# Performance work log

Hardware: AMD Instinct MI355X
Metric: run time of the kernel (lower is better)

## Reference

```python
import jax, jax.numpy as jnp
import numpy as np

X_DIM, H_DIM, Y_DIM, ROLLOUT = 256, 2048, 256, 4096


def setup_inputs() -> dict:
    key = jax.random.key(0)
    ks = jax.random.split(key, 6)
    inp = {
        "x": jax.random.normal(ks[0], (1, ROLLOUT, X_DIM), dtype=jnp.float32),
        "h": jnp.zeros((H_DIM,), dtype=jnp.float32),
        "Wc": jax.random.normal(ks[1], (X_DIM + H_DIM, H_DIM), dtype=jnp.float32) * 0.01,
        "Wu": jax.random.normal(ks[2], (X_DIM + H_DIM, H_DIM), dtype=jnp.float32) * 0.01,
        "Wr": jax.random.normal(ks[3], (X_DIM + H_DIM, H_DIM), dtype=jnp.float32) * 0.01,
        "bc": jnp.zeros((H_DIM,), dtype=jnp.float32),
        "bu": jnp.zeros((H_DIM,), dtype=jnp.float32),
        "br": jnp.zeros((H_DIM,), dtype=jnp.float32),
        "Wh_y": jax.random.normal(ks[4], (H_DIM, Y_DIM), dtype=jnp.float32) * 0.01,
        "by": jnp.zeros((Y_DIM,), dtype=jnp.float32),
    }
    return inp


def reference(x, h, Wc, Wu, Wr, bc, bu, br, Wh_y, by):
    xs = x[0]  # [T, x_dim]

    def step(hid, xt):
        xc = jnp.concatenate([xt, hid])                      # [x_dim + h_dim]
        Lu = jax.nn.sigmoid(xc @ Wu + bu)                    # update gate
        Lr = jax.nn.sigmoid(xc @ Wr + br)                    # reset gate
        xr = jnp.concatenate([xt, hid * Lr])
        c_tilda = jnp.tanh(xr @ Wc + bc)
        h_new = c_tilda * Lu + hid * (1.0 - Lu)
        y = h_new @ Wh_y + by
        return h_new, y

    h_fin, ys = jax.lax.scan(step, h, xs)  # ys: [T, y_dim]
    return ys, h_fin
```

## Files before the change

kernel.cpp:

```cpp
#include <hip/hip_runtime.h>
#include <hip/hip_bf16.h>

#define TSTEPS 4096
#define XD 256
#define HD 2048
#define YD 256
#define KD 2304
#define NWG 256
#define NT 512

#define WU_OFF 0
#define WR_OFF (8*KD*2)
#define WC_OFF (16*KD*2)
#define WY_OFF (24*KD*2)
#define HBUF_OFF (WY_OFF + HD*4)
#define ZBUF_OFF (HBUF_OFF + HD*4)
#define RED_OFF (ZBUF_OFF + HD*4)
#define LDS_BYTES (RED_OFF + 256)

#define HGO_U32 0
#define RGO_U32 2048
#define HB0_OFF 16384
#define HB1_OFF 49152
#define RB0_OFF 81920
#define RB1_OFF 114688
#define WS_ZERO_BYTES 147456
#define LSTRIDE 32

__device__ __forceinline__ float bflo(unsigned u){ return __uint_as_float(u << 16); }
__device__ __forceinline__ float bfhi(unsigned u){ return __uint_as_float(u & 0xffff0000u); }
__device__ __forceinline__ unsigned short f2bf(float f){
  unsigned b = __float_as_uint(f);
  b += 0x7fffu + ((b >> 16) & 1u);
  return (unsigned short)(b >> 16);
}
__device__ __forceinline__ float sigmoidf_(float x){ return 1.0f / (1.0f + __expf(-x)); }

__device__ __forceinline__ void storetag(float* p, float v, unsigned tag){
  unsigned b = (__float_as_uint(v) & ~3u) | tag;
  __hip_atomic_store((unsigned*)p, b, __ATOMIC_RELAXED, __HIP_MEMORY_SCOPE_AGENT);
}
__device__ __forceinline__ void flagst(unsigned* p, unsigned v){
  __hip_atomic_store(p, v, __ATOMIC_RELAXED, __HIP_MEMORY_SCOPE_AGENT);
}
__device__ __forceinline__ void spinflag(const unsigned* p, unsigned epoch, long* budget){
  while (__hip_atomic_load(p, __ATOMIC_RELAXED, __HIP_MEMORY_SCOPE_AGENT) < epoch) {
    if (--(*budget) < 0) break;
    __builtin_amdgcn_s_sleep(1);
  }
}

__device__ __forceinline__ void polline32(const float4* p, unsigned tag, long* budget,
                                          float4& r0, float4& r1){
  for (;;) {
    asm volatile("global_load_dwordx4 %0, %2, off sc1\n\t"
                 "global_load_dwordx4 %1, %2, off offset:16 sc1\n\t"
                 "s_waitcnt vmcnt(0)"
                 : "=v"(r0), "=v"(r1) : "v"(p) : "memory");
    unsigned m = (__float_as_uint(r0.x)^tag) | (__float_as_uint(r0.y)^tag)
               | (__float_as_uint(r0.z)^tag) | (__float_as_uint(r0.w)^tag)
               | (__float_as_uint(r1.x)^tag) | (__float_as_uint(r1.y)^tag)
               | (__float_as_uint(r1.z)^tag) | (__float_as_uint(r1.w)^tag);
    if ((m & 3u) == 0u) return;
    if (--(*budget) < 0) return;
    __builtin_amdgcn_s_sleep(1);
  }
}

__device__ __forceinline__ float4 cohload16(const float4* p){
  float4 r;
  asm volatile("global_load_dwordx4 %0, %1, off sc1\n\t"
               "s_waitcnt vmcnt(0)"
               : "=v"(r) : "v"(p) : "memory");
  return r;
}

template<int I0, int I1, int STRIDE>
__device__ __forceinline__ void dotacc(const float* v, const unsigned short* wcol,
                                       int lane, float4& acc){
  #pragma unroll
  for (int i = I0; i < I1; ++i) {
    int k = 4 * (lane + STRIDE * i);
    float4 vv = *(const float4*)(v + k);
    uint2  wq = *(const uint2*)(wcol + k);
    acc.x = fmaf(vv.x, bflo(wq.x), acc.x);
    acc.y = fmaf(vv.y, bfhi(wq.x), acc.y);
    acc.z = fmaf(vv.z, bflo(wq.y), acc.z);
    acc.w = fmaf(vv.w, bfhi(wq.y), acc.w);
  }
}
__device__ __forceinline__ void xpart(const float4 xq, const unsigned short* wcol,
                                      int l6, float4& acc){
  uint2 wq = *(const uint2*)(wcol + 4*l6);
  acc.x = fmaf(xq.x, bflo(wq.x), acc.x);
  acc.y = fmaf(xq.y, bfhi(wq.x), acc.y);
  acc.z = fmaf(xq.z, bflo(wq.y), acc.z);
  acc.w = fmaf(xq.w, bfhi(wq.y), acc.w);
}
__device__ __forceinline__ float redux64(float4 a){
  float s = (a.x + a.y) + (a.z + a.w);
  s += __shfl_xor(s, 32); s += __shfl_xor(s, 16); s += __shfl_xor(s, 8);
  s += __shfl_xor(s, 4);  s += __shfl_xor(s, 2);  s += __shfl_xor(s, 1);
  return s;
}

extern "C" __global__ void __launch_bounds__(NT)
gru_persistent(const float* __restrict__ x,  const float* __restrict__ h0,
               const float* __restrict__ Wc, const float* __restrict__ Wu,
               const float* __restrict__ Wr, const float* __restrict__ bc,
               const float* __restrict__ bu, const float* __restrict__ br,
               const float* __restrict__ Wy, const float* __restrict__ by,
               float* __restrict__ out, unsigned* wsu)
{
  extern __shared__ char smem[];
  unsigned short* wuS = (unsigned short*)(smem + WU_OFF);
  unsigned short* wrS = (unsigned short*)(smem + WR_OFF);
  unsigned short* wcS = (unsigned short*)(smem + WC_OFF);
  float* wyS   = (float*)(smem + WY_OFF);
  float* hbufS = (float*)(smem + HBUF_OFF);
  float* zbufS = (float*)(smem + ZBUF_OFF);
  float* red   = (float*)(smem + RED_OFF);

  unsigned* hgo = wsu + HGO_U32;
  unsigned* rgo = wsu + RGO_U32;
  float* hb[2] = { (float*)((char*)wsu + HB0_OFF), (float*)((char*)wsu + HB1_OFF) };
  float* rb[2] = { (float*)((char*)wsu + RB0_OFF), (float*)((char*)wsu + RB1_OFF) };

  const int wg = blockIdx.x, tid = threadIdx.x;
  const int col0 = 8 * wg;

  for (int idx = tid; idx < 8*KD; idx += NT) {
    int c = idx & 7, k = idx >> 3;
    size_t g = (size_t)k * HD + col0 + c;
    wuS[c*KD + k] = f2bf(Wu[g]);
    wrS[c*KD + k] = f2bf(Wr[g]);
    wcS[c*KD + k] = f2bf(Wc[g]);
  }
  for (int k = tid; k < HD; k += NT) wyS[k] = Wy[(size_t)k * YD + wg];
  if (tid < 8) {
    red[16+tid] = bu[col0+tid];
    red[24+tid] = br[col0+tid];
    red[32+tid] = bc[col0+tid];
    red[56+tid] = h0[col0+tid];
  }
  if (tid == 0) red[40] = by[wg];
  __syncthreads();

  long budget = 20000000;

  const int w  = tid >> 6, l6 = tid & 63;
  const int goline = ((wg & 7) << 3) + w;
  const int sw = tid >> 1, half = tid & 1;
  const int gidx = sw * (LSTRIDE/4) + half;
  const unsigned short* ucol = wuS + w * KD;
  const unsigned short* rcol = wrS + w * KD;
  const unsigned short* ccol = wcS + w * KD;

  float4 xq = ((const float4*)x)[l6];
  float ureg = 0.f;

  auto window = [&](int t){
    float4 au = make_float4(0.f, 0.f, 0.f, 0.f);
    xpart(xq, ucol, l6, au);
    dotacc<1, 9, 64>(hbufS - XD, ucol, l6, au);
    ureg = sigmoidf_(redux64(au) + red[16 + w]);
    int k = 256 * w + 4 * l6;
    float4 hv4 = *(const float4*)(hbufS + k);
    float4 wy4 = *(const float4*)(wyS + k);
    float ys = fmaf(hv4.x, wy4.x, fmaf(hv4.y, wy4.y, fmaf(hv4.z, wy4.z, hv4.w * wy4.w)));
    ys += __shfl_xor(ys, 32); ys += __shfl_xor(ys, 16); ys += __shfl_xor(ys, 8);
    ys += __shfl_xor(ys, 4);  ys += __shfl_xor(ys, 2);  ys += __shfl_xor(ys, 1);
    if (l6 == 0) red[8 + w] = ys;
    if (t + 1 < TSTEPS) xq = ((const float4*)(x + (size_t)(t+1) * XD))[l6];
  };

  for (int t = 0; t < TSTEPS; ++t) {
    float4 a1 = make_float4(0.f, 0.f, 0.f, 0.f);
    xpart(xq, rcol, l6, a1);

    if (t == 0) {
      ((float4*)hbufS)[tid] = ((const float4*)h0)[tid];
      __syncthreads();
    } else if (wg == 0) {
      if (tid < NWG) {
        float4 r0, r1;
        polline32((const float4*)hb[(t+1)&1] + tid*(LSTRIDE/4),
                  (unsigned)(t & 3), &budget, r0, r1);
        ((float4*)hbufS)[2*tid]   = r0;
        ((float4*)hbufS)[2*tid+1] = r1;
      }
      __syncthreads();
      if (tid < 64) flagst(hgo + tid*32, (unsigned)t);
    } else {
      if (l6 == 0) spinflag(hgo + goline*32, (unsigned)t, &budget);
      float4 hv = cohload16((const float4*)hb[(t+1)&1] + gidx);
      ((float4*)hbufS)[tid] = hv;
      __syncthreads();
    }

    dotacc<1, 9, 64>(hbufS - XD, rcol, l6, a1);
    {
      float s = redux64(a1);
      if (l6 == 0)
        storetag(rb[t&1] + wg*LSTRIDE + w,
                 sigmoidf_(s + red[24 + w]) * red[56 + w],
                 (unsigned)((t+1) & 3));
    }

    float4 a2 = make_float4(0.f, 0.f, 0.f, 0.f);
    xpart(xq, ccol, l6, a2);

    if (wg == 0) {
      if (tid < NWG) {
        float4 r0, r1;
        polline32((const float4*)rb[t&1] + tid*(LSTRIDE/4),
                  (unsigned)((t+1) & 3), &budget, r0, r1);
        ((float4*)zbufS)[2*tid]   = r0;
        ((float4*)zbufS)[2*tid+1] = r1;
      }
      __syncthreads();
      if (tid < 64) flagst(rgo + tid*32, (unsigned)(t+1));
      window(t);
      __syncthreads();
    } else {
      window(t);
      if (l6 == 0) spinflag(rgo + goline*32, (unsigned)(t+1), &budget);
      float4 rv = cohload16((const float4*)rb[t&1] + gidx);
      ((float4*)zbufS)[tid] = rv;
      __syncthreads();
    }

    if (tid == 0 && t > 0) {
      float y = red[8]+red[9]+red[10]+red[11]+red[12]+red[13]+red[14]+red[15] + red[40];
      out[(size_t)(t-1) * YD + wg] = y;
    }

    dotacc<1, 9, 64>(zbufS - XD, ccol, l6, a2);
    {
      float s = redux64(a2);
      if (l6 == 0) {
        float cc = tanhf(s + red[32 + w]);
        float hp = red[56 + w];
        float hn = cc * ureg + hp * (1.0f - ureg);
        red[56 + w] = hn;
        storetag(hb[t&1] + wg*LSTRIDE + w, hn,
                 (unsigned)((t+1) & 3));
      }
    }
  }

  if (wg == 0) {
    if (tid < NWG) {
      float4 r0, r1;
      polline32((const float4*)hb[(TSTEPS-1)&1] + tid*(LSTRIDE/4),
                (unsigned)(TSTEPS & 3), &budget, r0, r1);
      ((float4*)hbufS)[2*tid]   = r0;
      ((float4*)hbufS)[2*tid+1] = r1;
    }
    __syncthreads();
    if (tid < 64) flagst(hgo + tid*32, (unsigned)TSTEPS);
  } else {
    if (l6 == 0) spinflag(hgo + goline*32, (unsigned)TSTEPS, &budget);
    float4 hv = cohload16((const float4*)hb[(TSTEPS-1)&1] + gidx);
    ((float4*)hbufS)[tid] = hv;
    __syncthreads();
  }
  {
    int k = 256 * w + 4 * l6;
    float4 hv4 = *(const float4*)(hbufS + k);
    float4 wy4 = *(const float4*)(wyS + k);
    float ys = fmaf(hv4.x, wy4.x, fmaf(hv4.y, wy4.y, fmaf(hv4.z, wy4.z, hv4.w * wy4.w)));
    ys += __shfl_xor(ys, 32); ys += __shfl_xor(ys, 16); ys += __shfl_xor(ys, 8);
    ys += __shfl_xor(ys, 4);  ys += __shfl_xor(ys, 2);  ys += __shfl_xor(ys, 1);
    if (l6 == 0) red[8 + w] = ys;
  }
  __syncthreads();
  if (tid == 0) {
    float y = red[8]+red[9]+red[10]+red[11]+red[12]+red[13]+red[14]+red[15] + red[40];
    out[(size_t)(TSTEPS-1) * YD + wg] = y;
  }
  if (tid < 8) out[(size_t)TSTEPS * YD + col0 + tid] = red[56 + tid];
}

extern "C" void kernel_launch(void* const* d_in, const int* in_sizes, int n_in,
                              void* d_out, int out_size, void* d_ws, size_t ws_size,
                              hipStream_t stream) {
  const float* x  = (const float*)d_in[0];
  const float* h0 = (const float*)d_in[1];
  const float* Wc = (const float*)d_in[2];
  const float* Wu = (const float*)d_in[3];
  const float* Wr = (const float*)d_in[4];
  const float* bc = (const float*)d_in[5];
  const float* bu = (const float*)d_in[6];
  const float* br = (const float*)d_in[7];
  const float* Wy = (const float*)d_in[8];
  const float* by = (const float*)d_in[9];
  float* out = (float*)d_out;
  unsigned* wsu = (unsigned*)d_ws;

  (void)hipFuncSetAttribute((const void*)gru_persistent,
                            hipFuncAttributeMaxDynamicSharedMemorySize, LDS_BYTES);
  (void)hipMemsetAsync(d_ws, 0, WS_ZERO_BYTES, stream);
  gru_persistent<<<dim3(NWG), dim3(NT), LDS_BYTES, stream>>>(
      x, h0, Wc, Wu, Wr, bc, bu, br, Wy, by, out, wsu);
}
```

Baseline: 24.29 ms.

## Replace go-flag barrier with tagged dense gather buffers polled per chunk

Workgroup 0 still gathers the tagged partial h and r values from the strided per-workgroup lines. It now republishes them into dense, tag-carrying buffers, and the other workgroups poll their own 16-byte chunk directly instead of spinning on a separate go flag and then loading. This removes one flag store/load round trip and a __syncthreads from the critical path of each step. In exchange every consumer thread polls global memory, which raises coherent-memory polling traffic, and correctness relies on the low-bit tags surviving the relay.

```diff
diff --git a/kernel.cpp b/kernel.cpp
--- a/kernel.cpp
+++ b/kernel.cpp
@@ -18,13 +18,15 @@
 #define RED_OFF (ZBUF_OFF + HD*4)
 #define LDS_BYTES (RED_OFF + 256)
 
-#define HGO_U32 0
-#define RGO_U32 2048
-#define HB0_OFF 16384
-#define HB1_OFF 49152
-#define RB0_OFF 81920
-#define RB1_OFF 114688
-#define WS_ZERO_BYTES 147456
+#define HP0_OFF 0
+#define HP1_OFF 32768
+#define ZP0_OFF 65536
+#define ZP1_OFF 98304
+#define HD0_OFF 131072
+#define HD1_OFF 139264
+#define ZD0_OFF 147456
+#define ZD1_OFF 155648
+#define WS_ZERO_BYTES 163840
 #define LSTRIDE 32
 
 __device__ __forceinline__ float bflo(unsigned u){ return __uint_as_float(u << 16); }
@@ -40,14 +42,17 @@
   unsigned b = (__float_as_uint(v) & ~3u) | tag;
   __hip_atomic_store((unsigned*)p, b, __ATOMIC_RELAXED, __HIP_MEMORY_SCOPE_AGENT);
 }
-__device__ __forceinline__ void flagst(unsigned* p, unsigned v){
-  __hip_atomic_store(p, v, __ATOMIC_RELAXED, __HIP_MEMORY_SCOPE_AGENT);
-}
-__device__ __forceinline__ void spinflag(const unsigned* p, unsigned epoch, long* budget){
-  while (__hip_atomic_load(p, __ATOMIC_RELAXED, __HIP_MEMORY_SCOPE_AGENT) < epoch) {
-    if (--(*budget) < 0) break;
-    __builtin_amdgcn_s_sleep(1);
-  }
+
+__device__ __forceinline__ void stchunk32(float* p, float4 a, float4 b){
+  unsigned* q = (unsigned*)p;
+  __hip_atomic_store(q+0, __float_as_uint(a.x), __ATOMIC_RELAXED, __HIP_MEMORY_SCOPE_AGENT);
+  __hip_atomic_store(q+1, __float_as_uint(a.y), __ATOMIC_RELAXED, __HIP_MEMORY_SCOPE_AGENT);
+  __hip_atomic_store(q+2, __float_as_uint(a.z), __ATOMIC_RELAXED, __HIP_MEMORY_SCOPE_AGENT);
+  __hip_atomic_store(q+3, __float_as_uint(a.w), __ATOMIC_RELAXED, __HIP_MEMORY_SCOPE_AGENT);
+  __hip_atomic_store(q+4, __float_as_uint(b.x), __ATOMIC_RELAXED, __HIP_MEMORY_SCOPE_AGENT);
+  __hip_atomic_store(q+5, __float_as_uint(b.y), __ATOMIC_RELAXED, __HIP_MEMORY_SCOPE_AGENT);
+  __hip_atomic_store(q+6, __float_as_uint(b.z), __ATOMIC_RELAXED, __HIP_MEMORY_SCOPE_AGENT);
+  __hip_atomic_store(q+7, __float_as_uint(b.w), __ATOMIC_RELAXED, __HIP_MEMORY_SCOPE_AGENT);
 }
 
 __device__ __forceinline__ void polline32(const float4* p, unsigned tag, long* budget,
@@ -67,12 +72,18 @@
   }
 }
 
-__device__ __forceinline__ float4 cohload16(const float4* p){
-  float4 r;
-  asm volatile("global_load_dwordx4 %0, %1, off sc1\n\t"
-               "s_waitcnt vmcnt(0)"
-               : "=v"(r) : "v"(p) : "memory");
-  return r;
+__device__ __forceinline__ float4 pollchunk16(const float4* p, unsigned tag, long* budget){
+  for (;;) {
+    float4 r;
+    asm volatile("global_load_dwordx4 %0, %1, off sc1\n\t"
+                 "s_waitcnt vmcnt(0)"
+                 : "=v"(r) : "v"(p) : "memory");
+    unsigned m = (__float_as_uint(r.x)^tag) | (__float_as_uint(r.y)^tag)
+               | (__float_as_uint(r.z)^tag) | (__float_as_uint(r.w)^tag);
+    if ((m & 3u) == 0u) return r;
+    if (--(*budget) < 0) return r;
+    __builtin_amdgcn_s_sleep(1);
+  }
 }
 
 template<int I0, int I1, int STRIDE>
@@ -121,10 +132,10 @@
   float* zbufS = (float*)(smem + ZBUF_OFF);
   float* red   = (float*)(smem + RED_OFF);
 
-  unsigned* hgo = wsu + HGO_U32;
-  unsigned* rgo = wsu + RGO_U32;
-  float* hb[2] = { (float*)((char*)wsu + HB0_OFF), (float*)((char*)wsu + HB1_OFF) };
-  float* rb[2] = { (float*)((char*)wsu + RB0_OFF), (float*)((char*)wsu + RB1_OFF) };
+  float* hp[2]  = { (float*)((char*)wsu + HP0_OFF), (float*)((char*)wsu + HP1_OFF) };
+  float* zp[2]  = { (float*)((char*)wsu + ZP0_OFF), (float*)((char*)wsu + ZP1_OFF) };
+  float* hdg[2] = { (float*)((char*)wsu + HD0_OFF), (float*)((char*)wsu + HD1_OFF) };
+  float* zdg[2] = { (float*)((char*)wsu + ZD0_OFF), (float*)((char*)wsu + ZD1_OFF) };
 
   const int wg = blockIdx.x, tid = threadIdx.x;
   const int col0 = 8 * wg;
@@ -149,9 +160,6 @@
   long budget = 20000000;
 
   const int w  = tid >> 6, l6 = tid & 63;
-  const int goline = ((wg & 7) << 3) + w;
-  const int sw = tid >> 1, half = tid & 1;
-  const int gidx = sw * (LSTRIDE/4) + half;
   const unsigned short* ucol = wuS + w * KD;
   const unsigned short* rcol = wrS + w * KD;
   const unsigned short* ccol = wcS + w * KD;
@@ -184,16 +192,16 @@
     } else if (wg == 0) {
       if (tid < NWG) {
         float4 r0, r1;
-        polline32((const float4*)hb[(t+1)&1] + tid*(LSTRIDE/4),
+        polline32((const float4*)hp[(t+1)&1] + tid*(LSTRIDE/4),
                   (unsigned)(t & 3), &budget, r0, r1);
+        stchunk32(hdg[(t+1)&1] + 8*tid, r0, r1);
         ((float4*)hbufS)[2*tid]   = r0;
         ((float4*)hbufS)[2*tid+1] = r1;
       }
       __syncthreads();
-      if (tid < 64) flagst(hgo + tid*32, (unsigned)t);
     } else {
-      if (l6 == 0) spinflag(hgo + goline*32, (unsigned)t, &budget);
-      float4 hv = cohload16((const float4*)hb[(t+1)&1] + gidx);
+      float4 hv = pollchunk16((const float4*)hdg[(t+1)&1] + tid,
+                              (unsigned)(t & 3), &budget);
       ((float4*)hbufS)[tid] = hv;
       __syncthreads();
     }
@@ -202,7 +210,7 @@
     {
       float s = redux64(a1);
       if (l6 == 0)
-        storetag(rb[t&1] + wg*LSTRIDE + w,
+        storetag(zp[t&1] + wg*LSTRIDE + w,
                  sigmoidf_(s + red[24 + w]) * red[56 + w],
                  (unsigned)((t+1) & 3));
     }
@@ -213,20 +221,19 @@
     if (wg == 0) {
       if (tid < NWG) {
         float4 r0, r1;
-        polline32((const float4*)rb[t&1] + tid*(LSTRIDE/4),
+        polline32((const float4*)zp[t&1] + tid*(LSTRIDE/4),
                   (unsigned)((t+1) & 3), &budget, r0, r1);
+        stchunk32(zdg[t&1] + 8*tid, r0, r1);
         ((float4*)zbufS)[2*tid]   = r0;
         ((float4*)zbufS)[2*tid+1] = r1;
       }
-      __syncthreads();
-      if (tid < 64) flagst(rgo + tid*32, (unsigned)(t+1));
       window(t);
       __syncthreads();
     } else {
       window(t);
-      if (l6 == 0) spinflag(rgo + goline*32, (unsigned)(t+1), &budget);
-      float4 rv = cohload16((const float4*)rb[t&1] + gidx);
-      ((float4*)zbufS)[tid] = rv;
+      float4 zv = pollchunk16((const float4*)zdg[t&1] + tid,
+                              (unsigned)((t+1) & 3), &budget);
+      ((float4*)zbufS)[tid] = zv;
       __syncthreads();
     }
 
@@ -240,10 +247,10 @@
       float s = redux64(a2);
       if (l6 == 0) {
         float cc = tanhf(s + red[32 + w]);
-        float hp = red[56 + w];
-        float hn = cc * ureg + hp * (1.0f - ureg);
+        float hp_ = red[56 + w];
+        float hn = cc * ureg + hp_ * (1.0f - ureg);
         red[56 + w] = hn;
-        storetag(hb[t&1] + wg*LSTRIDE + w, hn,
+        storetag(hp[t&1] + wg*LSTRIDE + w, hn,
                  (unsigned)((t+1) & 3));
       }
     }
@@ -252,16 +259,16 @@
   if (wg == 0) {
     if (tid < NWG) {
       float4 r0, r1;
-      polline32((const float4*)hb[(TSTEPS-1)&1] + tid*(LSTRIDE/4),
+      polline32((const float4*)hp[(TSTEPS+1)&1] + tid*(LSTRIDE/4),
                 (unsigned)(TSTEPS & 3), &budget, r0, r1);
+      stchunk32(hdg[(TSTEPS+1)&1] + 8*tid, r0, r1);
       ((float4*)hbufS)[2*tid]   = r0;
       ((float4*)hbufS)[2*tid+1] = r1;
     }
     __syncthreads();
-    if (tid < 64) flagst(hgo + tid*32, (unsigned)TSTEPS);
   } else {
-    if (l6 == 0) spinflag(hgo + goline*32, (unsigned)TSTEPS, &budget);
-    float4 hv = cohload16((const float4*)hb[(TSTEPS-1)&1] + gidx);
+    float4 hv = pollchunk16((const float4*)hdg[(TSTEPS+1)&1] + tid,
+                            (unsigned)(TSTEPS & 3), &budget);
     ((float4*)hbufS)[tid] = hv;
     __syncthreads();
   }
```

After: 74.13 ms. +205.2%, slower.
